# Performance work log

Hardware: AMD Instinct MI355X
Metric: run time of the kernel (lower is better)

The kernel has to match this reference:

```python
import jax, jax.numpy as jnp
import numpy as np

B, N, T = 8192, 100, 64  # batch, ROI nodes, BOLD timepoints/features
GCN_DIMS = [(T, 32), (32, 16), (16, 8), (8, 4), (4, 2)]
EPS = 1e-5


def _kaiming(key, fout, fin):
    return jax.random.normal(key, (fout, fin), jnp.float32) * np.float32(np.sqrt(2.0 / fin))


def setup_inputs() -> dict:
    key = jax.random.key(0)
    ks = jax.random.split(key, 10)
    inp = {"BOLD_signals": jax.random.normal(ks[0], (B, N, T), jnp.float32)}
    inp["Wq"] = _kaiming(ks[1], 32, 64); inp["bq"] = jnp.zeros((32,), jnp.float32)
    inp["Wk"] = _kaiming(ks[2], 32, 64); inp["bk"] = jnp.zeros((32,), jnp.float32)
    inp["Wv"] = _kaiming(ks[3], 32, 64); inp["bv"] = jnp.zeros((32,), jnp.float32)
    for i, (fin, fout) in enumerate(GCN_DIMS):
        inp[f"W{i+1}"] = _kaiming(ks[4 + i], fout, fin)
        inp[f"b{i+1}"] = jnp.zeros((fout,), jnp.float32)
    inp["Wf"] = _kaiming(ks[9], 2, 200); inp["bf"] = jnp.zeros((2,), jnp.float32)
    return inp


def _corrcoef_batched(feat):
    # feat: [B, N, D]; rows are variables -> [B, N, N] correlation (torch.corrcoef, clipped)
    xc = feat - feat.mean(axis=-1, keepdims=True)
    cov = jnp.einsum('bnd,bmd->bnm', xc, xc)  # unnormalized; divisor cancels
    d = jnp.sqrt(jnp.einsum('bnn->bn', cov))
    corr = cov / (d[:, :, None] * d[:, None, :])
    return jnp.clip(corr, -1.0, 1.0)


def _batchnorm_nodes(h):
    # BatchNorm1d(100) on [B, 100, C]: normalize per node over (batch, feature) dims;
    # gamma=1, beta=0 per the module's constant init; training-mode batch stats.
    mean = h.mean(axis=(0, 2), keepdims=True)
    var = ((h - mean) ** 2).mean(axis=(0, 2), keepdims=True)
    return (h - mean) * jax.lax.rsqrt(var + EPS)


def _gcn(corr, h, W, b):
    z = jnp.einsum('bnm,bmf->bnf', corr, h) @ W.T + b
    return jnp.tanh(_batchnorm_nodes(z))


def reference(BOLD_signals, Wq, bq, Wk, bk, Wv, bv,
              W1, b1, W2, b2, W3, b3, W4, b4, W5, b5, Wf, bf):
    x = BOLD_signals
    Q = x @ Wq.T + bq
    K = x @ Wk.T + bk
    V = x @ Wv.T + bv
    A = jax.nn.softmax(jnp.einsum('bnd,bmd->bnm', Q, K) / 32.0, axis=2)
    feat = jnp.einsum('bnm,bmd->bnd', A, V)  # [B, N, 32]
    corr = _corrcoef_batched(feat)           # [B, N, N]
    h = x
    for (W, b) in [(W1, b1), (W2, b2), (W3, b3), (W4, b4), (W5, b5)]:
        h = _gcn(corr, h, W, b)
    out = h.reshape(h.shape[0], -1) @ Wf.T + bf  # [B, 2]
    return out
```

## Files before the change

### kernel.cpp

```cpp
#include <hip/hip_runtime.h>
#include <hip/hip_bf16.h>


typedef unsigned int u32;
typedef unsigned short u16;
typedef float f32x4 __attribute__((ext_vector_type(4)));
typedef short s16x8 __attribute__((ext_vector_type(8)));

__device__ __forceinline__ f32x4 mfma16(s16x8 a, s16x8 b, f32x4 c) {
  return __builtin_amdgcn_mfma_f32_16x16x32_bf16(a, b, c, 0, 0, 0);
}
__device__ __forceinline__ u16 f2b(float f) {
  __hip_bfloat16 h = __float2bfloat16(f);
  u16 u; __builtin_memcpy(&u, &h, 2); return u;
}
__device__ __forceinline__ float b2f(u16 u) { return __uint_as_float((u32)u << 16); }
__device__ __forceinline__ float blo(u32 u) { return __uint_as_float(u << 16); }
__device__ __forceinline__ float bhi(u32 u) { return __uint_as_float(u & 0xffff0000u); }
__device__ __forceinline__ u32 pack_hi2(float a, float b) { return (u32)f2b(a) | ((u32)f2b(b) << 16); }
__device__ __forceinline__ u32 pack_lo2(float a, float b) {
  return (u32)f2b(a - b2f(f2b(a))) | ((u32)f2b(b - b2f(f2b(b))) << 16);
}
__device__ __forceinline__ float fast_tanh(float x) {
  float e = __expf(2.0f * x);
  return 1.0f - 2.0f * __builtin_amdgcn_rcpf(e + 1.0f);
}

#define KA_XHI   0
#define KA_XLO   8064
#define KA_WHI   16128
#define KA_WLO   25344
#define KA_AHI   0
#define KA_ALO   15232
#define KA_CHI   0
#define KA_CLO   15232
#define KA_Q     34560
#define KA_K     39040
#define KA_VT    43520
#define KA_T0H   47872
#define KA_T0L   52224
#define KA_SX    72
#define KA_ASX   136
#define KA_QSX   40
#define KA_SMEM  113152

__global__ __launch_bounds__(512, 2) void ka_kernel(
    const float* __restrict__ x,
    const float* __restrict__ Wq, const float* __restrict__ bq,
    const float* __restrict__ Wk, const float* __restrict__ bk,
    const float* __restrict__ Wv, const float* __restrict__ bv,
    const float* __restrict__ W1, const float* __restrict__ b1,
    __hip_bfloat16* __restrict__ corr_g,
    float* __restrict__ z1g,
    float* __restrict__ stats1)
{
  __shared__ __align__(16) char smem[KA_SMEM];
  u16* S16 = (u16*)smem;
  const int b = blockIdx.x, tid = threadIdx.x;
  const int w = tid >> 6, l = tid & 63, l15 = l & 15, g = l >> 4;
  const f32x4 zero4 = {0.f, 0.f, 0.f, 0.f};

  {
    const float2* xg2 = (const float2*)(x + (size_t)b * 6400);
    for (int i = tid; i < 112 * 32; i += 512) {
      int r = i >> 5, c2 = i & 31;
      float vx = 0.f, vy = 0.f;
      if (r < 100) { float2 v = xg2[r * 32 + c2]; vx = v.x; vy = v.y; }
      *(u32*)&S16[KA_XHI + r * KA_SX + c2 * 2] = pack_hi2(vx, vy);
      *(u32*)&S16[KA_XLO + r * KA_SX + c2 * 2] = pack_lo2(vx, vy);
    }
    for (int i = tid; i < 128 * 32; i += 512) {
      int r = i >> 5, c2 = i & 31;
      const float* Wp = (r < 32) ? Wq : (r < 64) ? Wk : (r < 96) ? Wv : W1;
      float2 v = ((const float2*)Wp)[(r & 31) * 32 + c2];
      *(u32*)&S16[KA_WHI + r * KA_SX + c2 * 2] = pack_hi2(v.x, v.y);
      *(u32*)&S16[KA_WLO + r * KA_SX + c2 * 2] = pack_lo2(v.x, v.y);
    }
    for (int i = tid; i < 1152; i += 512) {
      int arr = i / 384, rem = i - arr * 384;
      int r = rem / 12, c = rem - r * 12;
      int base = (arr == 0) ? KA_VT : (arr == 1) ? KA_T0H : KA_T0L;
      *(u32*)&S16[base + r * KA_ASX + 112 + c * 2] = 0;
    }
  }
  __syncthreads();

  {
    const int mi = w >> 1;
    const int j = 16 * (w & 1) + l15;
    float bias = 0.f;
    if (mi == 0) bias = bq[j]; else if (mi == 1) bias = bk[j]; else if (mi == 2) bias = bv[j];
    for (int tm = 0; tm < 7; ++tm) {
      f32x4 acc = zero4;
#pragma unroll
      for (int kt = 0; kt < 2; ++kt) {
        s16x8 ah = *(const s16x8*)&S16[KA_XHI + (16 * tm + l15) * KA_SX + g * 8 + kt * 32];
        s16x8 al = *(const s16x8*)&S16[KA_XLO + (16 * tm + l15) * KA_SX + g * 8 + kt * 32];
        s16x8 bh = *(const s16x8*)&S16[KA_WHI + (16 * w + l15) * KA_SX + g * 8 + kt * 32];
        s16x8 bl = *(const s16x8*)&S16[KA_WLO + (16 * w + l15) * KA_SX + g * 8 + kt * 32];
        acc = mfma16(al, bh, acc);
        acc = mfma16(ah, bl, acc);
        acc = mfma16(ah, bh, acc);
      }
      const int row0 = 16 * tm + 4 * g;
#pragma unroll
      for (int r = 0; r < 4; ++r) {
        int row = row0 + r;
        float v = acc[r] + bias;
        u16 hv = f2b(v);
        if (mi == 0)      S16[KA_Q  + row * KA_QSX + j] = hv;
        else if (mi == 1) S16[KA_K  + row * KA_QSX + j] = hv;
        else if (mi == 2) S16[KA_VT + j * KA_ASX + row] = hv;
        else {
          S16[KA_T0H + j * KA_ASX + row] = hv;
          S16[KA_T0L + j * KA_ASX + row] = f2b(v - b2f(hv));
        }
      }
    }
  }
  __syncthreads();

  {
    for (int i = tid; i < 2688; i += 512) {
      int arr = i / 1344, rem = i - arr * 1344;
      int r = rem / 12, c = rem - r * 12;
      *(u32*)&S16[(arr ? KA_ALO : KA_AHI) + r * KA_ASX + 112 + c * 2] = 0;
    }
    if (w < 7) {
      const int tm = w;
      s16x8 aq = *(const s16x8*)&S16[KA_Q + (16 * tm + l15) * KA_QSX + g * 8];
      f32x4 sc[7];
#pragma unroll
      for (int tn = 0; tn < 7; ++tn) {
        s16x8 bb = *(const s16x8*)&S16[KA_K + (16 * tn + l15) * KA_QSX + g * 8];
        sc[tn] = mfma16(aq, bb, zero4);
      }
      const int row0 = 16 * tm + 4 * g;
#pragma unroll
      for (int r = 0; r < 4; ++r) {
        const int row = row0 + r;
        float v[7];
#pragma unroll
        for (int tn = 0; tn < 7; ++tn) v[tn] = sc[tn][r];
        if (l15 >= 4) v[6] = -3.0e38f;
        float m = v[0];
#pragma unroll
        for (int tn = 1; tn < 7; ++tn) m = fmaxf(m, v[tn]);
#pragma unroll
        for (int off = 1; off < 16; off <<= 1) m = fmaxf(m, __shfl_xor(m, off, 16));
        float e[7], s = 0.f;
#pragma unroll
        for (int tn = 0; tn < 7; ++tn) { e[tn] = __expf((v[tn] - m) * 0.03125f); s += e[tn]; }
#pragma unroll
        for (int off = 1; off < 16; off <<= 1) s += __shfl_xor(s, off, 16);
        float rr = __builtin_amdgcn_rcpf(s);
        bool ok = row < 100;
#pragma unroll
        for (int tn = 0; tn < 7; ++tn) {
          float a = ok ? e[tn] * rr : 0.f;
          u16 ah = f2b(a);
          S16[KA_AHI + row * KA_ASX + 16 * tn + l15] = ah;
          S16[KA_ALO + row * KA_ASX + 16 * tn + l15] = f2b(a - b2f(ah));
        }
      }
    }
  }
  __syncthreads();

  if (w < 7) {
    const int tm = w;
    f32x4 f0 = zero4, f1 = zero4;
#pragma unroll
    for (int kt = 0; kt < 4; ++kt) {
      s16x8 ah  = *(const s16x8*)&S16[KA_AHI + (16 * tm + l15) * KA_ASX + g * 8 + kt * 32];
      s16x8 al  = *(const s16x8*)&S16[KA_ALO + (16 * tm + l15) * KA_ASX + g * 8 + kt * 32];
      s16x8 b0  = *(const s16x8*)&S16[KA_VT + l15 * KA_ASX + g * 8 + kt * 32];
      s16x8 b1v = *(const s16x8*)&S16[KA_VT + (16 + l15) * KA_ASX + g * 8 + kt * 32];
      f0 = mfma16(al, b0, f0);  f0 = mfma16(ah, b0, f0);
      f1 = mfma16(al, b1v, f1); f1 = mfma16(ah, b1v, f1);
    }
    const int row0 = 16 * tm + 4 * g;
#pragma unroll
    for (int r = 0; r < 4; ++r) {
      float v0 = f0[r], v1 = f1[r];
      float s = v0 + v1;
#pragma unroll
      for (int off = 1; off < 16; off <<= 1) s += __shfl_xor(s, off, 16);
      float mean = s * 0.03125f;
      float xc0 = v0 - mean, xc1 = v1 - mean;
      float q = xc0 * xc0 + xc1 * xc1;
#pragma unroll
      for (int off = 1; off < 16; off <<= 1) q += __shfl_xor(q, off, 16);
      float inv = rsqrtf(q + 1e-30f);
      const int row = row0 + r;
      float c0 = xc0 * inv, c1 = xc1 * inv;
      u16 h0 = f2b(c0), h1 = f2b(c1);
      S16[KA_Q + row * KA_QSX + l15]      = h0;
      S16[KA_Q + row * KA_QSX + 16 + l15] = h1;
      S16[KA_K + row * KA_QSX + l15]      = f2b(c0 - b2f(h0));
      S16[KA_K + row * KA_QSX + 16 + l15] = f2b(c1 - b2f(h1));
    }
  }
  __syncthreads();

  if (w < 7) {
    u16* cgu = (u16*)(corr_g + (size_t)b * 10000);
    const int tm = w;
    s16x8 ah = *(const s16x8*)&S16[KA_Q + (16 * tm + l15) * KA_QSX + g * 8];
    s16x8 al = *(const s16x8*)&S16[KA_K + (16 * tm + l15) * KA_QSX + g * 8];
    const int row0 = 16 * tm + 4 * g;
#pragma unroll
    for (int tn = 0; tn < 7; ++tn) {
      s16x8 bh = *(const s16x8*)&S16[KA_Q + (16 * tn + l15) * KA_QSX + g * 8];
      s16x8 bl = *(const s16x8*)&S16[KA_K + (16 * tn + l15) * KA_QSX + g * 8];
      f32x4 c = mfma16(al, bh, zero4);
      c = mfma16(ah, bl, c);
      c = mfma16(ah, bh, c);
      const int col = 16 * tn + l15;
#pragma unroll
      for (int r = 0; r < 4; ++r) {
        float d = fminf(1.f, fmaxf(-1.f, c[r]));
        u16 ch = f2b(d);
        const int row = row0 + r;
        S16[KA_CHI + row * KA_ASX + col] = ch;
        S16[KA_CLO + row * KA_ASX + col] = f2b(d - b2f(ch));
        if (row < 100 && col < 100) cgu[row * 100 + col] = ch;
      }
    }
  }
  __syncthreads();

  if (w < 7) {
    const int tm = w;
    float bj0 = b1[l15], bj1 = b1[16 + l15];
    float* zo = z1g + (size_t)b * 3200;
    f32x4 z0 = zero4, z1v = zero4;
#pragma unroll
    for (int kt = 0; kt < 4; ++kt) {
      s16x8 a_h = *(const s16x8*)&S16[KA_CHI + (16 * tm + l15) * KA_ASX + g * 8 + kt * 32];
      s16x8 a_l = *(const s16x8*)&S16[KA_CLO + (16 * tm + l15) * KA_ASX + g * 8 + kt * 32];
      s16x8 b0h = *(const s16x8*)&S16[KA_T0H + l15 * KA_ASX + g * 8 + kt * 32];
      s16x8 b0l = *(const s16x8*)&S16[KA_T0L + l15 * KA_ASX + g * 8 + kt * 32];
      s16x8 b1h = *(const s16x8*)&S16[KA_T0H + (16 + l15) * KA_ASX + g * 8 + kt * 32];
      s16x8 b1l = *(const s16x8*)&S16[KA_T0L + (16 + l15) * KA_ASX + g * 8 + kt * 32];
      z0 = mfma16(a_l, b0h, z0);  z0 = mfma16(a_h, b0l, z0);  z0 = mfma16(a_h, b0h, z0);
      z1v = mfma16(a_l, b1h, z1v); z1v = mfma16(a_h, b1l, z1v); z1v = mfma16(a_h, b1h, z1v);
    }
    const int row0 = 16 * tm + 4 * g;
#pragma unroll
    for (int r = 0; r < 4; ++r) {
      const int row = row0 + r;
      float v0 = z0[r] + bj0, v1 = z1v[r] + bj1;
      if (row < 100) { zo[row * 32 + l15] = v0; zo[row * 32 + 16 + l15] = v1; }
      float s = v0 + v1, ss = v0 * v0 + v1 * v1;
#pragma unroll
      for (int off = 1; off < 16; off <<= 1) {
        s += __shfl_xor(s, off, 16); ss += __shfl_xor(ss, off, 16);
      }
      if (row < 100 && l15 == 0) { atomicAdd(&stats1[row], s); atomicAdd(&stats1[100 + row], ss); }
    }
  }
}

template<int FIN, int FOUT>
__global__ __launch_bounds__(256, 2) void kb_kernel(
    const float* __restrict__ zin,
    const __hip_bfloat16* __restrict__ corr_g,
    const float* __restrict__ W, const float* __restrict__ bias,
    const float* __restrict__ stats_in, float* __restrict__ stats_out,
    float* __restrict__ zout)
{
  constexpr int LOGF  = (FOUT == 16) ? 4 : (FOUT == 8) ? 3 : (FOUT == 4) ? 2 : 1;
  constexpr int LOGFI = (FIN == 32) ? 5 : (FIN == 16) ? 4 : (FIN == 8) ? 3 : 2;
  constexpr int RP = 256 / FOUT;
  constexpr int NR = (100 + RP - 1) / RP;

  __shared__ float mS[100], vS[100];
  __shared__ float hL[100 * 33];
  __shared__ float tL[100 * (FOUT + 1)];
  __shared__ __align__(16) float clL[100 * 104];

  const int b = blockIdx.x, tid = threadIdx.x;

  {
    const u32* cgu = (const u32*)(corr_g + (size_t)b * 10000);
    for (int u = tid; u < 5000; u += 256) {
      int n = (u * 5243) >> 18;
      int mm = (u - n * 50) << 1;
      u32 cc = cgu[u];
      clL[n * 104 + mm]     = blo(cc);
      clL[n * 104 + mm + 1] = bhi(cc);
    }
  }
  if (tid < 100) {
    float cnt  = 8192.0f * (float)FIN;
    float mean = stats_in[tid] / cnt;
    float var  = stats_in[100 + tid] / cnt - mean * mean;
    mS[tid] = mean;
    vS[tid] = rsqrtf(var + 1e-5f);
  }
  __syncthreads();

  {
    const float4* zb4 = (const float4*)(zin + (size_t)b * 100 * FIN);
    for (int i4 = tid; i4 < 25 * FIN; i4 += 256) {
      int n = i4 >> (LOGFI - 2);
      int c = (i4 << 2) & (FIN - 1);
      float4 z = zb4[i4];
      float mn = mS[n], iv = vS[n];
      hL[n * 33 + c + 0] = fast_tanh((z.x - mn) * iv);
      hL[n * 33 + c + 1] = fast_tanh((z.y - mn) * iv);
      hL[n * 33 + c + 2] = fast_tanh((z.z - mn) * iv);
      hL[n * 33 + c + 3] = fast_tanh((z.w - mn) * iv);
    }
  }
  __syncthreads();

  const int j  = tid & (FOUT - 1);
  const int nb = tid >> LOGF;

  {
    float wreg[FIN];
#pragma unroll
    for (int c = 0; c < FIN; ++c) wreg[c] = W[j * FIN + c];
#pragma unroll
    for (int k = 0; k < NR; ++k) {
      int n = nb + k * RP;
      if (n < 100) {
        float a = 0.f;
#pragma unroll
        for (int c = 0; c < FIN; ++c) a = fmaf(hL[n * 33 + c], wreg[c], a);
        tL[n * (FOUT + 1) + j] = a;
      }
    }
  }
  __syncthreads();

  {
    float acc[NR];
    float bj = bias[j];
#pragma unroll
    for (int k = 0; k < NR; ++k) acc[k] = bj;
    int nrow[NR];
#pragma unroll
    for (int k = 0; k < NR; ++k) nrow[k] = min(nb + k * RP, 99);
    const float4* c4 = (const float4*)clL;
#pragma unroll 5
    for (int m4 = 0; m4 < 25; ++m4) {
      float ta = tL[(m4 * 4 + 0) * (FOUT + 1) + j];
      float tb = tL[(m4 * 4 + 1) * (FOUT + 1) + j];
      float tc = tL[(m4 * 4 + 2) * (FOUT + 1) + j];
      float td = tL[(m4 * 4 + 3) * (FOUT + 1) + j];
#pragma unroll
      for (int k = 0; k < NR; ++k) {
        float4 c = c4[nrow[k] * 26 + m4];
        acc[k] = fmaf(c.x, ta, fmaf(c.y, tb, fmaf(c.z, tc, fmaf(c.w, td, acc[k]))));
      }
    }
    float* zo = zout + (size_t)b * 100 * FOUT;
#pragma unroll
    for (int k = 0; k < NR; ++k) {
      int n = nb + k * RP;
      if (n < 100) {
        float v = acc[k];
        zo[n * FOUT + j] = v;
        float s = v, ss = v * v;
#pragma unroll
        for (int off = FOUT >> 1; off; off >>= 1) {
          s  += __shfl_xor(s, off, FOUT);
          ss += __shfl_xor(ss, off, FOUT);
        }
        if (j == 0) {
          atomicAdd(&stats_out[n], s);
          atomicAdd(&stats_out[100 + n], ss);
        }
      }
    }
  }
}

__global__ __launch_bounds__(256) void kf_kernel(
    const float* __restrict__ z5, const float* __restrict__ stats5,
    const float* __restrict__ Wf, const float* __restrict__ bfv,
    float* __restrict__ out)
{
  __shared__ float mS[100], vS[100];
  const int tid = threadIdx.x;
  if (tid < 100) {
    float cnt  = 8192.0f * 2.0f;
    float mean = stats5[tid] / cnt;
    float var  = stats5[100 + tid] / cnt - mean * mean;
    mS[tid] = mean;
    vS[tid] = rsqrtf(var + 1e-5f);
  }
  __syncthreads();
  const int wvid = tid >> 6, lane = tid & 63;
  const int b = blockIdx.x * 4 + wvid;
  const float* zb = z5 + (size_t)b * 200;
  float a0 = 0.f, a1 = 0.f;
#pragma unroll
  for (int p = 0; p < 4; ++p) {
    int jj = lane + p * 64;
    if (jj < 200) {
      int n = jj >> 1;
      float hv = fast_tanh((zb[jj] - mS[n]) * vS[n]);
      a0 = fmaf(hv, Wf[jj], a0);
      a1 = fmaf(hv, Wf[200 + jj], a1);
    }
  }
#pragma unroll
  for (int off = 32; off; off >>= 1) {
    a0 += __shfl_xor(a0, off, 64);
    a1 += __shfl_xor(a1, off, 64);
  }
  if (lane == 0) {
    out[b * 2 + 0] = a0 + bfv[0];
    out[b * 2 + 1] = a1 + bfv[1];
  }
}

extern "C" void kernel_launch(void* const* d_in, const int* in_sizes, int n_in,
                              void* d_out, int out_size, void* d_ws, size_t ws_size,
                              hipStream_t stream)
{
  const float* x  = (const float*)d_in[0];
  const float* Wq = (const float*)d_in[1];
  const float* bq = (const float*)d_in[2];
  const float* Wk = (const float*)d_in[3];
  const float* bk = (const float*)d_in[4];
  const float* Wv = (const float*)d_in[5];
  const float* bv = (const float*)d_in[6];
  const float* W1 = (const float*)d_in[7];
  const float* b1 = (const float*)d_in[8];
  const float* W2 = (const float*)d_in[9];
  const float* b2 = (const float*)d_in[10];
  const float* W3 = (const float*)d_in[11];
  const float* b3 = (const float*)d_in[12];
  const float* W4 = (const float*)d_in[13];
  const float* b4 = (const float*)d_in[14];
  const float* W5 = (const float*)d_in[15];
  const float* b5 = (const float*)d_in[16];
  const float* Wf = (const float*)d_in[17];
  const float* bf = (const float*)d_in[18];
  float* out = (float*)d_out;

  char* ws = (char*)d_ws;
  const size_t NEED = 321130400ull;
  if (ws_size < NEED) return;

  __hip_bfloat16* corr_g = (__hip_bfloat16*)ws;
  float* zA    = (float*)(ws + 163840000ull);
  float* zB    = (float*)(ws + 268697600ull);
  float* stats = (float*)(ws + 321126400ull);

  (void)hipMemsetAsync(stats, 0, 5 * 200 * sizeof(float), stream);

  ka_kernel<<<8192, 512, 0, stream>>>(x, Wq, bq, Wk, bk, Wv, bv, W1, b1,
                                      corr_g, zA, stats);
  kb_kernel<32, 16><<<8192, 256, 0, stream>>>(zA, corr_g, W2, b2, stats,       stats + 200, zB);
  kb_kernel<16,  8><<<8192, 256, 0, stream>>>(zB, corr_g, W3, b3, stats + 200, stats + 400, zA);
  kb_kernel< 8,  4><<<8192, 256, 0, stream>>>(zA, corr_g, W4, b4, stats + 400, stats + 600, zB);
  kb_kernel< 4,  2><<<8192, 256, 0, stream>>>(zB, corr_g, W5, b5, stats + 600, stats + 800, zA);
  kf_kernel<<<2048, 256, 0, stream>>>(zA, stats + 800, Wf, bf, out);
}
```

Measured before the change: 4.019 ms.

## Shrink LDS footprint in fused attention/corr kernel and store bf16 corr in GCN layers

New measurement: 3.984 ms. Within noise of the previous version (-0.9%).

```diff
diff --git a/kernel.cpp b/kernel.cpp
--- a/kernel.cpp
+++ b/kernel.cpp
@@ -26,25 +26,15 @@
   return 1.0f - 2.0f * __builtin_amdgcn_rcpf(e + 1.0f);
 }
 
-#define KA_XHI   0
-#define KA_XLO   8064
-#define KA_WHI   16128
-#define KA_WLO   25344
-#define KA_AHI   0
-#define KA_ALO   15232
-#define KA_CHI   0
-#define KA_CLO   15232
-#define KA_Q     34560
-#define KA_K     39040
-#define KA_VT    43520
-#define KA_T0H   47872
-#define KA_T0L   52224
-#define KA_SX    72
-#define KA_ASX   136
-#define KA_QSX   40
-#define KA_SMEM  113152
-
-__global__ __launch_bounds__(512, 2) void ka_kernel(
+#define KA_XLO_B  16128
+#define KA_Q_B    44800
+#define KA_K_B    52864
+#define KA_CHAT_B 44800
+#define KA_V_B    60928
+#define KA_T0_B   67728
+#define KA_SMEM_B 80928
+
+__global__ __launch_bounds__(512, 4) void ka_kernel(
     const float* __restrict__ x,
     const float* __restrict__ Wq, const float* __restrict__ bq,
     const float* __restrict__ Wk, const float* __restrict__ bk,
@@ -54,8 +44,16 @@
     float* __restrict__ z1g,
     float* __restrict__ stats1)
 {
-  __shared__ __align__(16) char smem[KA_SMEM];
-  u16* S16 = (u16*)smem;
+  __shared__ __align__(16) char smem[KA_SMEM_B];
+  u16*   xh   = (u16*)smem;
+  u16*   xl   = (u16*)(smem + KA_XLO_B);
+  float* Af   = (float*)smem;
+  u16*   Qs   = (u16*)(smem + KA_Q_B);
+  u16*   Ks   = (u16*)(smem + KA_K_B);
+  float* chat = (float*)(smem + KA_CHAT_B);
+  u16*   Vb   = (u16*)(smem + KA_V_B);
+  float* t0   = (float*)(smem + KA_T0_B);
+
   const int b = blockIdx.x, tid = threadIdx.x;
   const int w = tid >> 6, l = tid & 63, l15 = l & 15, g = l >> 4;
   const f32x4 zero4 = {0.f, 0.f, 0.f, 0.f};
@@ -66,102 +64,48 @@
       int r = i >> 5, c2 = i & 31;
       float vx = 0.f, vy = 0.f;
       if (r < 100) { float2 v = xg2[r * 32 + c2]; vx = v.x; vy = v.y; }
-      *(u32*)&S16[KA_XHI + r * KA_SX + c2 * 2] = pack_hi2(vx, vy);
-      *(u32*)&S16[KA_XLO + r * KA_SX + c2 * 2] = pack_lo2(vx, vy);
-    }
-    for (int i = tid; i < 128 * 32; i += 512) {
-      int r = i >> 5, c2 = i & 31;
-      const float* Wp = (r < 32) ? Wq : (r < 64) ? Wk : (r < 96) ? Wv : W1;
-      float2 v = ((const float2*)Wp)[(r & 31) * 32 + c2];
-      *(u32*)&S16[KA_WHI + r * KA_SX + c2 * 2] = pack_hi2(v.x, v.y);
-      *(u32*)&S16[KA_WLO + r * KA_SX + c2 * 2] = pack_lo2(v.x, v.y);
-    }
-    for (int i = tid; i < 1152; i += 512) {
-      int arr = i / 384, rem = i - arr * 384;
-      int r = rem / 12, c = rem - r * 12;
-      int base = (arr == 0) ? KA_VT : (arr == 1) ? KA_T0H : KA_T0L;
-      *(u32*)&S16[base + r * KA_ASX + 112 + c * 2] = 0;
-    }
-  }
-  __syncthreads();
-
-  {
-    const int mi = w >> 1;
-    const int j = 16 * (w & 1) + l15;
-    float bias = 0.f;
-    if (mi == 0) bias = bq[j]; else if (mi == 1) bias = bk[j]; else if (mi == 2) bias = bv[j];
+      ((u32*)xh)[r * 36 + c2] = pack_hi2(vx, vy);
+      ((u32*)xl)[r * 36 + c2] = pack_lo2(vx, vy);
+    }
+  }
+  __syncthreads();
+
+  {
+    const int mi = w >> 1, half = w & 1;
+    const int j = 16 * half + l15;
+    const float* Wp = (mi == 0) ? Wq : (mi == 1) ? Wk : (mi == 2) ? Wv : W1;
+    float bias = (mi == 0) ? bq[j] : (mi == 1) ? bk[j] : (mi == 2) ? bv[j] : 0.f;
+    s16x8 bh[2], bl[2];
+#pragma unroll
+    for (int kt = 0; kt < 2; ++kt) {
+      const float* wr = Wp + j * 64 + kt * 32 + g * 8;
+#pragma unroll
+      for (int e = 0; e < 8; ++e) {
+        float wv = wr[e];
+        u16 hh = f2b(wv);
+        bh[kt][e] = (short)hh;
+        bl[kt][e] = (short)f2b(wv - b2f(hh));
+      }
+    }
     for (int tm = 0; tm < 7; ++tm) {
       f32x4 acc = zero4;
 #pragma unroll
       for (int kt = 0; kt < 2; ++kt) {
-        s16x8 ah = *(const s16x8*)&S16[KA_XHI + (16 * tm + l15) * KA_SX + g * 8 + kt * 32];
-        s16x8 al = *(const s16x8*)&S16[KA_XLO + (16 * tm + l15) * KA_SX + g * 8 + kt * 32];
-        s16x8 bh = *(const s16x8*)&S16[KA_WHI + (16 * w + l15) * KA_SX + g * 8 + kt * 32];
-        s16x8 bl = *(const s16x8*)&S16[KA_WLO + (16 * w + l15) * KA_SX + g * 8 + kt * 32];
-        acc = mfma16(al, bh, acc);
-        acc = mfma16(ah, bl, acc);
-        acc = mfma16(ah, bh, acc);
+        s16x8 ah = *(const s16x8*)&xh[(16 * tm + l15) * 72 + kt * 32 + g * 8];
+        s16x8 al = *(const s16x8*)&xl[(16 * tm + l15) * 72 + kt * 32 + g * 8];
+        acc = mfma16(al, bh[kt], acc);
+        acc = mfma16(ah, bl[kt], acc);
+        acc = mfma16(ah, bh[kt], acc);
       }
       const int row0 = 16 * tm + 4 * g;
 #pragma unroll
       for (int r = 0; r < 4; ++r) {
         int row = row0 + r;
         float v = acc[r] + bias;
-        u16 hv = f2b(v);
-        if (mi == 0)      S16[KA_Q  + row * KA_QSX + j] = hv;
-        else if (mi == 1) S16[KA_K  + row * KA_QSX + j] = hv;
-        else if (mi == 2) S16[KA_VT + j * KA_ASX + row] = hv;
-        else {
-          S16[KA_T0H + j * KA_ASX + row] = hv;
-          S16[KA_T0L + j * KA_ASX + row] = f2b(v - b2f(hv));
-        }
-      }
-    }
-  }
-  __syncthreads();
-
-  {
-    for (int i = tid; i < 2688; i += 512) {
-      int arr = i / 1344, rem = i - arr * 1344;
-      int r = rem / 12, c = rem - r * 12;
-      *(u32*)&S16[(arr ? KA_ALO : KA_AHI) + r * KA_ASX + 112 + c * 2] = 0;
-    }
-    if (w < 7) {
-      const int tm = w;
-      s16x8 aq = *(const s16x8*)&S16[KA_Q + (16 * tm + l15) * KA_QSX + g * 8];
-      f32x4 sc[7];
-#pragma unroll
-      for (int tn = 0; tn < 7; ++tn) {
-        s16x8 bb = *(const s16x8*)&S16[KA_K + (16 * tn + l15) * KA_QSX + g * 8];
-        sc[tn] = mfma16(aq, bb, zero4);
-      }
-      const int row0 = 16 * tm + 4 * g;
-#pragma unroll
-      for (int r = 0; r < 4; ++r) {
-        const int row = row0 + r;
-        float v[7];
-#pragma unroll
-        for (int tn = 0; tn < 7; ++tn) v[tn] = sc[tn][r];
-        if (l15 >= 4) v[6] = -3.0e38f;
-        float m = v[0];
-#pragma unroll
-        for (int tn = 1; tn < 7; ++tn) m = fmaxf(m, v[tn]);
-#pragma unroll
-        for (int off = 1; off < 16; off <<= 1) m = fmaxf(m, __shfl_xor(m, off, 16));
-        float e[7], s = 0.f;
-#pragma unroll
-        for (int tn = 0; tn < 7; ++tn) { e[tn] = __expf((v[tn] - m) * 0.03125f); s += e[tn]; }
-#pragma unroll
-        for (int off = 1; off < 16; off <<= 1) s += __shfl_xor(s, off, 16);
-        float rr = __builtin_amdgcn_rcpf(s);
-        bool ok = row < 100;
-#pragma unroll
-        for (int tn = 0; tn < 7; ++tn) {
-          float a = ok ? e[tn] * rr : 0.f;
-          u16 ah = f2b(a);
-          S16[KA_AHI + row * KA_ASX + 16 * tn + l15] = ah;
-          S16[KA_ALO + row * KA_ASX + 16 * tn + l15] = f2b(a - b2f(ah));
-        }
+        if (mi == 0)      Qs[row * 36 + j] = f2b(v);
+        else if (mi == 1) Ks[row * 36 + j] = f2b(v);
+        else if (mi == 2) { if (row < 100) Vb[row * 34 + j] = f2b(v); }
+        else              { if (row < 100) t0[row * 33 + j] = v; }
       }
     }
   }
@@ -169,101 +113,160 @@
 
   if (w < 7) {
     const int tm = w;
-    f32x4 f0 = zero4, f1 = zero4;
-#pragma unroll
-    for (int kt = 0; kt < 4; ++kt) {
-      s16x8 ah  = *(const s16x8*)&S16[KA_AHI + (16 * tm + l15) * KA_ASX + g * 8 + kt * 32];
-      s16x8 al  = *(const s16x8*)&S16[KA_ALO + (16 * tm + l15) * KA_ASX + g * 8 + kt * 32];
-      s16x8 b0  = *(const s16x8*)&S16[KA_VT + l15 * KA_ASX + g * 8 + kt * 32];
-      s16x8 b1v = *(const s16x8*)&S16[KA_VT + (16 + l15) * KA_ASX + g * 8 + kt * 32];
-      f0 = mfma16(al, b0, f0);  f0 = mfma16(ah, b0, f0);
-      f1 = mfma16(al, b1v, f1); f1 = mfma16(ah, b1v, f1);
-    }
-    const int row0 = 16 * tm + 4 * g;
-#pragma unroll
-    for (int r = 0; r < 4; ++r) {
-      float v0 = f0[r], v1 = f1[r];
-      float s = v0 + v1;
-#pragma unroll
-      for (int off = 1; off < 16; off <<= 1) s += __shfl_xor(s, off, 16);
-      float mean = s * 0.03125f;
-      float xc0 = v0 - mean, xc1 = v1 - mean;
-      float q = xc0 * xc0 + xc1 * xc1;
-#pragma unroll
-      for (int off = 1; off < 16; off <<= 1) q += __shfl_xor(q, off, 16);
-      float inv = rsqrtf(q + 1e-30f);
-      const int row = row0 + r;
-      float c0 = xc0 * inv, c1 = xc1 * inv;
-      u16 h0 = f2b(c0), h1 = f2b(c1);
-      S16[KA_Q + row * KA_QSX + l15]      = h0;
-      S16[KA_Q + row * KA_QSX + 16 + l15] = h1;
-      S16[KA_K + row * KA_QSX + l15]      = f2b(c0 - b2f(h0));
-      S16[KA_K + row * KA_QSX + 16 + l15] = f2b(c1 - b2f(h1));
-    }
-  }
-  __syncthreads();
-
-  if (w < 7) {
-    u16* cgu = (u16*)(corr_g + (size_t)b * 10000);
-    const int tm = w;
-    s16x8 ah = *(const s16x8*)&S16[KA_Q + (16 * tm + l15) * KA_QSX + g * 8];
-    s16x8 al = *(const s16x8*)&S16[KA_K + (16 * tm + l15) * KA_QSX + g * 8];
-    const int row0 = 16 * tm + 4 * g;
+    s16x8 aq = *(const s16x8*)&Qs[(16 * tm + l15) * 36 + g * 8];
+    f32x4 sc[7];
 #pragma unroll
     for (int tn = 0; tn < 7; ++tn) {
-      s16x8 bh = *(const s16x8*)&S16[KA_Q + (16 * tn + l15) * KA_QSX + g * 8];
-      s16x8 bl = *(const s16x8*)&S16[KA_K + (16 * tn + l15) * KA_QSX + g * 8];
-      f32x4 c = mfma16(al, bh, zero4);
-      c = mfma16(ah, bl, c);
-      c = mfma16(ah, bh, c);
-      const int col = 16 * tn + l15;
-#pragma unroll
-      for (int r = 0; r < 4; ++r) {
-        float d = fminf(1.f, fmaxf(-1.f, c[r]));
-        u16 ch = f2b(d);
-        const int row = row0 + r;
-        S16[KA_CHI + row * KA_ASX + col] = ch;
-        S16[KA_CLO + row * KA_ASX + col] = f2b(d - b2f(ch));
-        if (row < 100 && col < 100) cgu[row * 100 + col] = ch;
-      }
-    }
-  }
-  __syncthreads();
-
-  if (w < 7) {
-    const int tm = w;
-    float bj0 = b1[l15], bj1 = b1[16 + l15];
-    float* zo = z1g + (size_t)b * 3200;
-    f32x4 z0 = zero4, z1v = zero4;
-#pragma unroll
-    for (int kt = 0; kt < 4; ++kt) {
-      s16x8 a_h = *(const s16x8*)&S16[KA_CHI + (16 * tm + l15) * KA_ASX + g * 8 + kt * 32];
-      s16x8 a_l = *(const s16x8*)&S16[KA_CLO + (16 * tm + l15) * KA_ASX + g * 8 + kt * 32];
-      s16x8 b0h = *(const s16x8*)&S16[KA_T0H + l15 * KA_ASX + g * 8 + kt * 32];
-      s16x8 b0l = *(const s16x8*)&S16[KA_T0L + l15 * KA_ASX + g * 8 + kt * 32];
-      s16x8 b1h = *(const s16x8*)&S16[KA_T0H + (16 + l15) * KA_ASX + g * 8 + kt * 32];
-      s16x8 b1l = *(const s16x8*)&S16[KA_T0L + (16 + l15) * KA_ASX + g * 8 + kt * 32];
-      z0 = mfma16(a_l, b0h, z0);  z0 = mfma16(a_h, b0l, z0);  z0 = mfma16(a_h, b0h, z0);
-      z1v = mfma16(a_l, b1h, z1v); z1v = mfma16(a_h, b1l, z1v); z1v = mfma16(a_h, b1h, z1v);
+      s16x8 bb = *(const s16x8*)&Ks[(16 * tn + l15) * 36 + g * 8];
+      sc[tn] = mfma16(aq, bb, zero4);
     }
     const int row0 = 16 * tm + 4 * g;
 #pragma unroll
     for (int r = 0; r < 4; ++r) {
       const int row = row0 + r;
-      float v0 = z0[r] + bj0, v1 = z1v[r] + bj1;
-      if (row < 100) { zo[row * 32 + l15] = v0; zo[row * 32 + 16 + l15] = v1; }
-      float s = v0 + v1, ss = v0 * v0 + v1 * v1;
-#pragma unroll
-      for (int off = 1; off < 16; off <<= 1) {
-        s += __shfl_xor(s, off, 16); ss += __shfl_xor(ss, off, 16);
-      }
-      if (row < 100 && l15 == 0) { atomicAdd(&stats1[row], s); atomicAdd(&stats1[100 + row], ss); }
+      float v[7];
+#pragma unroll
+      for (int tn = 0; tn < 7; ++tn) v[tn] = sc[tn][r];
+      if (l15 >= 4) v[6] = -3.0e38f;
+      float m = v[0];
+#pragma unroll
+      for (int tn = 1; tn < 7; ++tn) m = fmaxf(m, v[tn]);
+#pragma unroll
+      for (int off = 1; off < 16; off <<= 1) m = fmaxf(m, __shfl_xor(m, off, 16));
+      float e[7], s = 0.f;
+#pragma unroll
+      for (int tn = 0; tn < 7; ++tn) { e[tn] = __expf((v[tn] - m) * 0.03125f); s += e[tn]; }
+#pragma unroll
+      for (int off = 1; off < 16; off <<= 1) s += __shfl_xor(s, off, 16);
+      float rr = __builtin_amdgcn_rcpf(s);
+      bool ok = row < 100;
+#pragma unroll
+      for (int tn = 0; tn < 7; ++tn) {
+        int col = 16 * tn + l15;
+        float a = ok ? e[tn] * rr : 0.f;
+        if (col < 100) Af[row * 100 + col] = a;
+      }
+    }
+  }
+  __syncthreads();
+
+  {
+    const int j = tid & 31, gr = tid >> 5;
+    float fa[7];
+#pragma unroll
+    for (int k = 0; k < 7; ++k) fa[k] = 0.f;
+    const float4* A4 = (const float4*)Af;
+#pragma unroll 5
+    for (int m4 = 0; m4 < 25; ++m4) {
+      float v0 = b2f(Vb[(4 * m4 + 0) * 34 + j]);
+      float v1 = b2f(Vb[(4 * m4 + 1) * 34 + j]);
+      float v2 = b2f(Vb[(4 * m4 + 2) * 34 + j]);
+      float v3 = b2f(Vb[(4 * m4 + 3) * 34 + j]);
+#pragma unroll
+      for (int k = 0; k < 7; ++k) {
+        float4 a = A4[(gr + 16 * k) * 25 + m4];
+        fa[k] = fmaf(a.x, v0, fmaf(a.y, v1, fmaf(a.z, v2, fmaf(a.w, v3, fa[k]))));
+      }
+    }
+#pragma unroll
+    for (int k = 0; k < 7; ++k) {
+      int n = gr + 16 * k;
+      float vv = fa[k];
+      float s = vv;
+#pragma unroll
+      for (int off = 16; off; off >>= 1) s += __shfl_xor(s, off, 32);
+      float mean = s * 0.03125f;
+      float xc = vv - mean;
+      float q = xc * xc;
+#pragma unroll
+      for (int off = 16; off; off >>= 1) q += __shfl_xor(q, off, 32);
+      float inv = rsqrtf(q + 1e-30f);
+      if (n < 100) chat[n * 33 + j] = xc * inv;
+    }
+  }
+  __syncthreads();
+
+  {
+    float c0a[13], c1a[13];
+#pragma unroll
+    for (int k = 0; k < 13; ++k) { c0a[k] = 0.f; c1a[k] = 0.f; }
+    const float* ca = chat + l * 33;
+    const float* cb = chat + (l + 64) * 33;
+    const bool mok = l < 36;
+#pragma unroll 4
+    for (int t = 0; t < 32; ++t) {
+      float a = ca[t], bb2 = cb[t];
+#pragma unroll
+      for (int k = 0; k < 13; ++k) {
+        float q = chat[(w + 8 * k) * 33 + t];
+        c0a[k] = fmaf(q, a, c0a[k]);
+        c1a[k] = fmaf(q, bb2, c1a[k]);
+      }
+    }
+    u16* cgu = (u16*)(corr_g + (size_t)b * 10000);
+#pragma unroll
+    for (int k = 0; k < 13; ++k) {
+      int row = w + 8 * k;
+      if (row < 100) {
+        float d0 = fminf(1.f, fmaxf(-1.f, c0a[k]));
+        Af[row * 100 + l] = d0;
+        cgu[row * 100 + l] = f2b(d0);
+        if (mok) {
+          float d1 = fminf(1.f, fmaxf(-1.f, c1a[k]));
+          Af[row * 100 + 64 + l] = d1;
+          cgu[row * 100 + 64 + l] = f2b(d1);
+        }
+      }
+    }
+  }
+  __syncthreads();
+
+  {
+    const int j = tid & 31, gr = tid >> 5;
+    float acc[7];
+    float bj = b1[j];
+#pragma unroll
+    for (int k = 0; k < 7; ++k) acc[k] = bj;
+    int nrow[7];
+#pragma unroll
+    for (int k = 0; k < 7; ++k) nrow[k] = min(gr + 16 * k, 99);
+    const float4* c4 = (const float4*)Af;
+#pragma unroll 5
+    for (int m4 = 0; m4 < 25; ++m4) {
+      float ta = t0[(4 * m4 + 0) * 33 + j];
+      float tb = t0[(4 * m4 + 1) * 33 + j];
+      float tc = t0[(4 * m4 + 2) * 33 + j];
+      float td = t0[(4 * m4 + 3) * 33 + j];
+#pragma unroll
+      for (int k = 0; k < 7; ++k) {
+        float4 c = c4[nrow[k] * 25 + m4];
+        acc[k] = fmaf(c.x, ta, fmaf(c.y, tb, fmaf(c.z, tc, fmaf(c.w, td, acc[k]))));
+      }
+    }
+    float* zo = z1g + (size_t)b * 3200;
+#pragma unroll
+    for (int k = 0; k < 7; ++k) {
+      int n = gr + 16 * k;
+      if (n < 100) {
+        float v = acc[k];
+        zo[n * 32 + j] = v;
+        float s = v, ss = v * v;
+#pragma unroll
+        for (int off = 16; off; off >>= 1) {
+          s  += __shfl_xor(s, off, 32);
+          ss += __shfl_xor(ss, off, 32);
+        }
+        if (j == 0) {
+          atomicAdd(&stats1[n], s);
+          atomicAdd(&stats1[100 + n], ss);
+        }
+      }
     }
   }
 }
 
 template<int FIN, int FOUT>
-__global__ __launch_bounds__(256, 2) void kb_kernel(
+__global__ __launch_bounds__(256, 3) void kb_kernel(
     const float* __restrict__ zin,
     const __hip_bfloat16* __restrict__ corr_g,
     const float* __restrict__ W, const float* __restrict__ bias,
@@ -275,21 +278,19 @@
   constexpr int RP = 256 / FOUT;
   constexpr int NR = (100 + RP - 1) / RP;
 
+  __shared__ u32 clLu[100 * 52];
   __shared__ float mS[100], vS[100];
   __shared__ float hL[100 * 33];
   __shared__ float tL[100 * (FOUT + 1)];
-  __shared__ __align__(16) float clL[100 * 104];
 
   const int b = blockIdx.x, tid = threadIdx.x;
 
   {
     const u32* cgu = (const u32*)(corr_g + (size_t)b * 10000);
-    for (int u = tid; u < 5000; u += 256) {
-      int n = (u * 5243) >> 18;
-      int mm = (u - n * 50) << 1;
-      u32 cc = cgu[u];
-      clL[n * 104 + mm]     = blo(cc);
-      clL[n * 104 + mm + 1] = bhi(cc);
+    for (int i = tid; i < 5000; i += 256) {
+      int n = (i * 5243) >> 18;
+      int mm = i - n * 50;
+      clLu[n * 52 + mm] = cgu[i];
     }
   }
   if (tid < 100) {
@@ -344,7 +345,6 @@
     int nrow[NR];
 #pragma unroll
     for (int k = 0; k < NR; ++k) nrow[k] = min(nb + k * RP, 99);
-    const float4* c4 = (const float4*)clL;
 #pragma unroll 5
     for (int m4 = 0; m4 < 25; ++m4) {
       float ta = tL[(m4 * 4 + 0) * (FOUT + 1) + j];
@@ -353,8 +353,10 @@
       float td = tL[(m4 * 4 + 3) * (FOUT + 1) + j];
 #pragma unroll
       for (int k = 0; k < NR; ++k) {
-        float4 c = c4[nrow[k] * 26 + m4];
-        acc[k] = fmaf(c.x, ta, fmaf(c.y, tb, fmaf(c.z, tc, fmaf(c.w, td, acc[k]))));
+        u32 p0 = clLu[nrow[k] * 52 + 2 * m4];
+        u32 p1 = clLu[nrow[k] * 52 + 2 * m4 + 1];
+        acc[k] = fmaf(blo(p0), ta, fmaf(bhi(p0), tb,
+                 fmaf(blo(p1), tc, fmaf(bhi(p1), td, acc[k]))));
       }
     }
     float* zo = zout + (size_t)b * 100 * FOUT;
```

## Shrink shared memory in ka and kb kernels to raise occupancy

Applied to the files above, without the earlier changes.

New measurement: 3.858 ms. 1.04x faster.

```diff
diff --git a/kernel.cpp b/kernel.cpp
--- a/kernel.cpp
+++ b/kernel.cpp
@@ -26,25 +26,21 @@
   return 1.0f - 2.0f * __builtin_amdgcn_rcpf(e + 1.0f);
 }
 
-#define KA_XHI   0
-#define KA_XLO   8064
-#define KA_WHI   16128
-#define KA_WLO   25344
-#define KA_AHI   0
-#define KA_ALO   15232
-#define KA_CHI   0
-#define KA_CLO   15232
-#define KA_Q     34560
-#define KA_K     39040
-#define KA_VT    43520
-#define KA_T0H   47872
-#define KA_T0L   52224
-#define KA_SX    72
-#define KA_ASX   136
-#define KA_QSX   40
-#define KA_SMEM  113152
-
-__global__ __launch_bounds__(512, 2) void ka_kernel(
+#define KA_XHI_B   0
+#define KA_XLO_B   16128
+#define KA_A_B     0
+#define KA_QS_B    32256
+#define KA_KS_B    40320
+#define KA_CHH_B   32256
+#define KA_CHL_B   40320
+#define KA_VT_B    48384
+#define KA_CRH_B   0
+#define KA_CRL_B   30464
+#define KA_T0H_B   60928
+#define KA_T0L_B   69632
+#define KA_SMEM_B  78336
+
+__global__ __launch_bounds__(512, 4) void ka_kernel(
     const float* __restrict__ x,
     const float* __restrict__ Wq, const float* __restrict__ bq,
     const float* __restrict__ Wk, const float* __restrict__ bk,
@@ -54,11 +50,26 @@
     float* __restrict__ z1g,
     float* __restrict__ stats1)
 {
-  __shared__ __align__(16) char smem[KA_SMEM];
-  u16* S16 = (u16*)smem;
+  __shared__ __align__(16) char smem[KA_SMEM_B];
+  u16* xh  = (u16*)(smem + KA_XHI_B);
+  u16* xl  = (u16*)(smem + KA_XLO_B);
+  u16* A16 = (u16*)(smem + KA_A_B);
+  u16* Qs  = (u16*)(smem + KA_QS_B);
+  u16* Ks  = (u16*)(smem + KA_KS_B);
+  u16* chh = (u16*)(smem + KA_CHH_B);
+  u16* chl = (u16*)(smem + KA_CHL_B);
+  u16* Vt  = (u16*)(smem + KA_VT_B);
+  u16* crh = (u16*)(smem + KA_CRH_B);
+  u16* crl = (u16*)(smem + KA_CRL_B);
+  u16* t0h = (u16*)(smem + KA_T0H_B);
+  u16* t0l = (u16*)(smem + KA_T0L_B);
+
   const int b = blockIdx.x, tid = threadIdx.x;
-  const int w = tid >> 6, l = tid & 63, l15 = l & 15, g = l >> 4;
+  const int w = tid >> 6, l15 = tid & 15, g = (tid & 63) >> 4;
   const f32x4 zero4 = {0.f, 0.f, 0.f, 0.f};
+
+  float t0r[28];
+  float cr[7][4];
 
   {
     const float2* xg2 = (const float2*)(x + (size_t)b * 6400);
@@ -66,103 +77,93 @@
       int r = i >> 5, c2 = i & 31;
       float vx = 0.f, vy = 0.f;
       if (r < 100) { float2 v = xg2[r * 32 + c2]; vx = v.x; vy = v.y; }
-      *(u32*)&S16[KA_XHI + r * KA_SX + c2 * 2] = pack_hi2(vx, vy);
-      *(u32*)&S16[KA_XLO + r * KA_SX + c2 * 2] = pack_lo2(vx, vy);
-    }
-    for (int i = tid; i < 128 * 32; i += 512) {
-      int r = i >> 5, c2 = i & 31;
-      const float* Wp = (r < 32) ? Wq : (r < 64) ? Wk : (r < 96) ? Wv : W1;
-      float2 v = ((const float2*)Wp)[(r & 31) * 32 + c2];
-      *(u32*)&S16[KA_WHI + r * KA_SX + c2 * 2] = pack_hi2(v.x, v.y);
-      *(u32*)&S16[KA_WLO + r * KA_SX + c2 * 2] = pack_lo2(v.x, v.y);
-    }
-    for (int i = tid; i < 1152; i += 512) {
-      int arr = i / 384, rem = i - arr * 384;
-      int r = rem / 12, c = rem - r * 12;
-      int base = (arr == 0) ? KA_VT : (arr == 1) ? KA_T0H : KA_T0L;
-      *(u32*)&S16[base + r * KA_ASX + 112 + c * 2] = 0;
-    }
-  }
-  __syncthreads();
-
-  {
-    const int mi = w >> 1;
-    const int j = 16 * (w & 1) + l15;
-    float bias = 0.f;
-    if (mi == 0) bias = bq[j]; else if (mi == 1) bias = bk[j]; else if (mi == 2) bias = bv[j];
+      ((u32*)xh)[r * 36 + c2] = pack_hi2(vx, vy);
+      ((u32*)xl)[r * 36 + c2] = pack_lo2(vx, vy);
+    }
+    if (tid < 256) {
+      int j = tid >> 3, ii = tid & 7;
+      ((u32*)Vt)[j * 68 + 56 + ii] = 0;
+    }
+  }
+  __syncthreads();
+
+  {
+    const int mi = w >> 1, half = w & 1;
+    const int j = 16 * half + l15;
+    const float* Wp = (mi == 0) ? Wq : (mi == 1) ? Wk : (mi == 2) ? Wv : W1;
+    float bias = (mi == 0) ? bq[j] : (mi == 1) ? bk[j] : (mi == 2) ? bv[j] : 0.f;
+    s16x8 bhf[2], blf[2];
+#pragma unroll
+    for (int kt = 0; kt < 2; ++kt) {
+      const float* wr = Wp + j * 64 + kt * 32 + g * 8;
+#pragma unroll
+      for (int e = 0; e < 8; ++e) {
+        float wv = wr[e];
+        u16 hh = f2b(wv);
+        bhf[kt][e] = (short)hh;
+        blf[kt][e] = (short)f2b(wv - b2f(hh));
+      }
+    }
+#pragma unroll
     for (int tm = 0; tm < 7; ++tm) {
       f32x4 acc = zero4;
 #pragma unroll
       for (int kt = 0; kt < 2; ++kt) {
-        s16x8 ah = *(const s16x8*)&S16[KA_XHI + (16 * tm + l15) * KA_SX + g * 8 + kt * 32];
-        s16x8 al = *(const s16x8*)&S16[KA_XLO + (16 * tm + l15) * KA_SX + g * 8 + kt * 32];
-        s16x8 bh = *(const s16x8*)&S16[KA_WHI + (16 * w + l15) * KA_SX + g * 8 + kt * 32];
-        s16x8 bl = *(const s16x8*)&S16[KA_WLO + (16 * w + l15) * KA_SX + g * 8 + kt * 32];
-        acc = mfma16(al, bh, acc);
-        acc = mfma16(ah, bl, acc);
-        acc = mfma16(ah, bh, acc);
+        s16x8 ah = *(const s16x8*)&xh[(16 * tm + l15) * 72 + kt * 32 + g * 8];
+        s16x8 al = *(const s16x8*)&xl[(16 * tm + l15) * 72 + kt * 32 + g * 8];
+        acc = mfma16(al, bhf[kt], acc);
+        acc = mfma16(ah, blf[kt], acc);
+        acc = mfma16(ah, bhf[kt], acc);
       }
       const int row0 = 16 * tm + 4 * g;
 #pragma unroll
       for (int r = 0; r < 4; ++r) {
         int row = row0 + r;
         float v = acc[r] + bias;
-        u16 hv = f2b(v);
-        if (mi == 0)      S16[KA_Q  + row * KA_QSX + j] = hv;
-        else if (mi == 1) S16[KA_K  + row * KA_QSX + j] = hv;
-        else if (mi == 2) S16[KA_VT + j * KA_ASX + row] = hv;
-        else {
-          S16[KA_T0H + j * KA_ASX + row] = hv;
-          S16[KA_T0L + j * KA_ASX + row] = f2b(v - b2f(hv));
-        }
-      }
-    }
-  }
-  __syncthreads();
-
-  {
-    for (int i = tid; i < 2688; i += 512) {
-      int arr = i / 1344, rem = i - arr * 1344;
-      int r = rem / 12, c = rem - r * 12;
-      *(u32*)&S16[(arr ? KA_ALO : KA_AHI) + r * KA_ASX + 112 + c * 2] = 0;
-    }
-    if (w < 7) {
-      const int tm = w;
-      s16x8 aq = *(const s16x8*)&S16[KA_Q + (16 * tm + l15) * KA_QSX + g * 8];
-      f32x4 sc[7];
+        if (mi == 0)      Qs[row * 36 + j] = f2b(v);
+        else if (mi == 1) Ks[row * 36 + j] = f2b(v);
+        else if (mi == 2) Vt[j * 136 + row] = f2b(v);
+        else              t0r[tm * 4 + r] = v;
+      }
+    }
+  }
+  __syncthreads();
+
+  if (w < 7) {
+    const int tm = w;
+    s16x8 aq = *(const s16x8*)&Qs[(16 * tm + l15) * 36 + g * 8];
+    f32x4 sc[7];
+#pragma unroll
+    for (int tn = 0; tn < 7; ++tn) {
+      s16x8 bb = *(const s16x8*)&Ks[(16 * tn + l15) * 36 + g * 8];
+      sc[tn] = mfma16(aq, bb, zero4);
+    }
+    const int row0 = 16 * tm + 4 * g;
+#pragma unroll
+    for (int r = 0; r < 4; ++r) {
+      const int row = row0 + r;
+      float v[7];
+#pragma unroll
+      for (int tn = 0; tn < 7; ++tn) v[tn] = sc[tn][r];
+      if (l15 >= 4) v[6] = -3.0e38f;
+      float m = v[0];
+#pragma unroll
+      for (int tn = 1; tn < 7; ++tn) m = fmaxf(m, v[tn]);
+#pragma unroll
+      for (int off = 1; off < 16; off <<= 1) m = fmaxf(m, __shfl_xor(m, off, 16));
+      float e[7], s = 0.f;
+#pragma unroll
+      for (int tn = 0; tn < 7; ++tn) { e[tn] = __expf((v[tn] - m) * 0.03125f); s += e[tn]; }
+#pragma unroll
+      for (int off = 1; off < 16; off <<= 1) s += __shfl_xor(s, off, 16);
+      float rr = __builtin_amdgcn_rcpf(s);
+      bool ok = row < 100;
 #pragma unroll
       for (int tn = 0; tn < 7; ++tn) {
-        s16x8 bb = *(const s16x8*)&S16[KA_K + (16 * tn + l15) * KA_QSX + g * 8];
-        sc[tn] = mfma16(aq, bb, zero4);
-      }
-      const int row0 = 16 * tm + 4 * g;
-#pragma unroll
-      for (int r = 0; r < 4; ++r) {
-        const int row = row0 + r;
-        float v[7];
-#pragma unroll
-        for (int tn = 0; tn < 7; ++tn) v[tn] = sc[tn][r];
-        if (l15 >= 4) v[6] = -3.0e38f;
-        float m = v[0];
-#pragma unroll
-        for (int tn = 1; tn < 7; ++tn) m = fmaxf(m, v[tn]);
-#pragma unroll
-        for (int off = 1; off < 16; off <<= 1) m = fmaxf(m, __shfl_xor(m, off, 16));
-        float e[7], s = 0.f;
-#pragma unroll
-        for (int tn = 0; tn < 7; ++tn) { e[tn] = __expf((v[tn] - m) * 0.03125f); s += e[tn]; }
-#pragma unroll
-        for (int off = 1; off < 16; off <<= 1) s += __shfl_xor(s, off, 16);
-        float rr = __builtin_amdgcn_rcpf(s);
-        bool ok = row < 100;
-#pragma unroll
-        for (int tn = 0; tn < 7; ++tn) {
-          float a = ok ? e[tn] * rr : 0.f;
-          u16 ah = f2b(a);
-          S16[KA_AHI + row * KA_ASX + 16 * tn + l15] = ah;
-          S16[KA_ALO + row * KA_ASX + 16 * tn + l15] = f2b(a - b2f(ah));
-        }
-      }
+        float a = ok ? e[tn] * rr : 0.f;
+        A16[row * 136 + 16 * tn + l15] = f2b(a);
+      }
+      if (l15 < 8) ((u32*)A16)[row * 68 + 56 + l15] = 0;
     }
   }
   __syncthreads();
@@ -172,12 +173,11 @@
     f32x4 f0 = zero4, f1 = zero4;
 #pragma unroll
     for (int kt = 0; kt < 4; ++kt) {
-      s16x8 ah  = *(const s16x8*)&S16[KA_AHI + (16 * tm + l15) * KA_ASX + g * 8 + kt * 32];
-      s16x8 al  = *(const s16x8*)&S16[KA_ALO + (16 * tm + l15) * KA_ASX + g * 8 + kt * 32];
-      s16x8 b0  = *(const s16x8*)&S16[KA_VT + l15 * KA_ASX + g * 8 + kt * 32];
-      s16x8 b1v = *(const s16x8*)&S16[KA_VT + (16 + l15) * KA_ASX + g * 8 + kt * 32];
-      f0 = mfma16(al, b0, f0);  f0 = mfma16(ah, b0, f0);
-      f1 = mfma16(al, b1v, f1); f1 = mfma16(ah, b1v, f1);
+      s16x8 a   = *(const s16x8*)&A16[(16 * tm + l15) * 136 + kt * 32 + g * 8];
+      s16x8 b0  = *(const s16x8*)&Vt[l15 * 136 + kt * 32 + g * 8];
+      s16x8 b1v = *(const s16x8*)&Vt[(16 + l15) * 136 + kt * 32 + g * 8];
+      f0 = mfma16(a, b0, f0);
+      f1 = mfma16(a, b1v, f1);
     }
     const int row0 = 16 * tm + 4 * g;
 #pragma unroll
@@ -195,10 +195,10 @@
       const int row = row0 + r;
       float c0 = xc0 * inv, c1 = xc1 * inv;
       u16 h0 = f2b(c0), h1 = f2b(c1);
-      S16[KA_Q + row * KA_QSX + l15]      = h0;
-      S16[KA_Q + row * KA_QSX + 16 + l15] = h1;
-      S16[KA_K + row * KA_QSX + l15]      = f2b(c0 - b2f(h0));
-      S16[KA_K + row * KA_QSX + 16 + l15] = f2b(c1 - b2f(h1));
+      chh[row * 36 + l15]      = h0;
+      chh[row * 36 + 16 + l15] = h1;
+      chl[row * 36 + l15]      = f2b(c0 - b2f(h0));
+      chl[row * 36 + 16 + l15] = f2b(c1 - b2f(h1));
     }
   }
   __syncthreads();
@@ -206,13 +206,13 @@
   if (w < 7) {
     u16* cgu = (u16*)(corr_g + (size_t)b * 10000);
     const int tm = w;
-    s16x8 ah = *(const s16x8*)&S16[KA_Q + (16 * tm + l15) * KA_QSX + g * 8];
-    s16x8 al = *(const s16x8*)&S16[KA_K + (16 * tm + l15) * KA_QSX + g * 8];
+    s16x8 ah = *(const s16x8*)&chh[(16 * tm + l15) * 36 + g * 8];
+    s16x8 al = *(const s16x8*)&chl[(16 * tm + l15) * 36 + g * 8];
     const int row0 = 16 * tm + 4 * g;
 #pragma unroll
     for (int tn = 0; tn < 7; ++tn) {
-      s16x8 bh = *(const s16x8*)&S16[KA_Q + (16 * tn + l15) * KA_QSX + g * 8];
-      s16x8 bl = *(const s16x8*)&S16[KA_K + (16 * tn + l15) * KA_QSX + g * 8];
+      s16x8 bh = *(const s16x8*)&chh[(16 * tn + l15) * 36 + g * 8];
+      s16x8 bl = *(const s16x8*)&chl[(16 * tn + l15) * 36 + g * 8];
       f32x4 c = mfma16(al, bh, zero4);
       c = mfma16(ah, bl, c);
       c = mfma16(ah, bh, c);
@@ -220,11 +220,54 @@
 #pragma unroll
       for (int r = 0; r < 4; ++r) {
         float d = fminf(1.f, fmaxf(-1.f, c[r]));
-        u16 ch = f2b(d);
+        cr[tn][r] = d;
         const int row = row0 + r;
-        S16[KA_CHI + row * KA_ASX + col] = ch;
-        S16[KA_CLO + row * KA_ASX + col] = f2b(d - b2f(ch));
-        if (row < 100 && col < 100) cgu[row * 100 + col] = ch;
+        if (row < 100 && col < 100) cgu[row * 100 + col] = f2b(d);
+      }
+    }
+  }
+  __syncthreads();
+
+  {
+    if (w < 7) {
+      const int tm = w;
+      const int row0 = 16 * tm + 4 * g;
+#pragma unroll
+      for (int r = 0; r < 4; ++r) {
+        const int row = row0 + r;
+#pragma unroll
+        for (int tn = 0; tn < 7; ++tn) {
+          const int col = 16 * tn + l15;
+          float d = cr[tn][r];
+          u16 hh = f2b(d);
+          crh[row * 136 + col] = hh;
+          crl[row * 136 + col] = f2b(d - b2f(hh));
+        }
+        if (l15 < 8) {
+          ((u32*)crh)[row * 68 + 56 + l15] = 0;
+          ((u32*)crl)[row * 68 + 56 + l15] = 0;
+        }
+      }
+    }
+    if (w >= 6) {
+      const int j = 16 * (w & 1) + l15;
+#pragma unroll
+      for (int tm = 0; tm < 7; ++tm) {
+#pragma unroll
+        for (int r = 0; r < 4; ++r) {
+          int m = 16 * tm + 4 * g + r;
+          float v = t0r[tm * 4 + r];
+          u16 hh = f2b(v);
+          t0h[j * 136 + m] = hh;
+          t0l[j * 136 + m] = f2b(v - b2f(hh));
+        }
+      }
+      if (g == 0) {
+#pragma unroll
+        for (int ii = 0; ii < 8; ++ii) ((u32*)t0h)[j * 68 + 56 + ii] = 0;
+      } else if (g == 1) {
+#pragma unroll
+        for (int ii = 0; ii < 8; ++ii) ((u32*)t0l)[j * 68 + 56 + ii] = 0;
       }
     }
   }
@@ -237,12 +280,12 @@
     f32x4 z0 = zero4, z1v = zero4;
 #pragma unroll
     for (int kt = 0; kt < 4; ++kt) {
-      s16x8 a_h = *(const s16x8*)&S16[KA_CHI + (16 * tm + l15) * KA_ASX + g * 8 + kt * 32];
-      s16x8 a_l = *(const s16x8*)&S16[KA_CLO + (16 * tm + l15) * KA_ASX + g * 8 + kt * 32];
-      s16x8 b0h = *(const s16x8*)&S16[KA_T0H + l15 * KA_ASX + g * 8 + kt * 32];
-      s16x8 b0l = *(const s16x8*)&S16[KA_T0L + l15 * KA_ASX + g * 8 + kt * 32];
-      s16x8 b1h = *(const s16x8*)&S16[KA_T0H + (16 + l15) * KA_ASX + g * 8 + kt * 32];
-      s16x8 b1l = *(const s16x8*)&S16[KA_T0L + (16 + l15) * KA_ASX + g * 8 + kt * 32];
+      s16x8 a_h = *(const s16x8*)&crh[(16 * tm + l15) * 136 + kt * 32 + g * 8];
+      s16x8 a_l = *(const s16x8*)&crl[(16 * tm + l15) * 136 + kt * 32 + g * 8];
+      s16x8 b0h = *(const s16x8*)&t0h[l15 * 136 + kt * 32 + g * 8];
+      s16x8 b0l = *(const s16x8*)&t0l[l15 * 136 + kt * 32 + g * 8];
+      s16x8 b1h = *(const s16x8*)&t0h[(16 + l15) * 136 + kt * 32 + g * 8];
+      s16x8 b1l = *(const s16x8*)&t0l[(16 + l15) * 136 + kt * 32 + g * 8];
       z0 = mfma16(a_l, b0h, z0);  z0 = mfma16(a_h, b0l, z0);  z0 = mfma16(a_h, b0h, z0);
       z1v = mfma16(a_l, b1h, z1v); z1v = mfma16(a_h, b1l, z1v); z1v = mfma16(a_h, b1h, z1v);
     }
@@ -263,7 +306,7 @@
 }
 
 template<int FIN, int FOUT>
-__global__ __launch_bounds__(256, 2) void kb_kernel(
+__global__ __launch_bounds__(256, 3) void kb_kernel(
     const float* __restrict__ zin,
     const __hip_bfloat16* __restrict__ corr_g,
     const float* __restrict__ W, const float* __restrict__ bias,
@@ -275,21 +318,19 @@
   constexpr int RP = 256 / FOUT;
   constexpr int NR = (100 + RP - 1) / RP;
 
+  __shared__ u32 clLu[100 * 52];
   __shared__ float mS[100], vS[100];
   __shared__ float hL[100 * 33];
   __shared__ float tL[100 * (FOUT + 1)];
-  __shared__ __align__(16) float clL[100 * 104];
 
   const int b = blockIdx.x, tid = threadIdx.x;
 
   {
     const u32* cgu = (const u32*)(corr_g + (size_t)b * 10000);
-    for (int u = tid; u < 5000; u += 256) {
-      int n = (u * 5243) >> 18;
-      int mm = (u - n * 50) << 1;
-      u32 cc = cgu[u];
-      clL[n * 104 + mm]     = blo(cc);
-      clL[n * 104 + mm + 1] = bhi(cc);
+    for (int i = tid; i < 5000; i += 256) {
+      int n = (i * 5243) >> 18;
+      int mm = i - n * 50;
+      clLu[n * 52 + mm] = cgu[i];
     }
   }
   if (tid < 100) {
@@ -344,7 +385,6 @@
     int nrow[NR];
 #pragma unroll
     for (int k = 0; k < NR; ++k) nrow[k] = min(nb + k * RP, 99);
-    const float4* c4 = (const float4*)clL;
 #pragma unroll 5
     for (int m4 = 0; m4 < 25; ++m4) {
       float ta = tL[(m4 * 4 + 0) * (FOUT + 1) + j];
@@ -353,8 +393,10 @@
       float td = tL[(m4 * 4 + 3) * (FOUT + 1) + j];
 #pragma unroll
       for (int k = 0; k < NR; ++k) {
-        float4 c = c4[nrow[k] * 26 + m4];
-        acc[k] = fmaf(c.x, ta, fmaf(c.y, tb, fmaf(c.z, tc, fmaf(c.w, td, acc[k]))));
+        u32 p0 = clLu[nrow[k] * 52 + 2 * m4];
+        u32 p1 = clLu[nrow[k] * 52 + 2 * m4 + 1];
+        acc[k] = fmaf(blo(p0), ta, fmaf(bhi(p0), tb,
+                 fmaf(blo(p1), tc, fmaf(bhi(p1), td, acc[k]))));
       }
     }
     float* zo = zout + (size_t)b * 100 * FOUT;
```
